# Performance work log

Hardware: AMD Instinct MI355X
Metric: run time of the kernel (lower is better)

The kernel has to match this reference:

```python
import jax, jax.numpy as jnp
import numpy as np

D_MODEL = 256
D_INNER = 512   # expand * dim
D_STATE = 16
D_CONV = 4
DT_RANK = 16    # ceil(dim / 16)
PATCH = 64


def _silu(v):
    return v * jax.nn.sigmoid(v)


def _causal_dwconv(x, w, b):
    # x: (b, d, l); w: (d, 1, k) depthwise; causal left pad k-1
    y = jax.lax.conv_general_dilated(
        x, w, window_strides=(1,), padding=[(D_CONV - 1, 0)],
        feature_group_count=D_INNER, dimension_numbers=("NCH", "OIH", "NCH"))
    return y + b[None, :, None]


def _selective_scan(u, delta, A, Bm, Cm, Dp):
    # u, delta: (b, d, l); A: (d, n); Bm, Cm: (b, n, l)
    dA = jnp.exp(jnp.einsum("bdl,dn->lbdn", delta, A))
    dBu = jnp.einsum("bdl,bnl,bdl->lbdn", delta, Bm, u)
    Ct = jnp.transpose(Cm, (2, 0, 1))  # (l, b, n)

    def step(h, inp):
        dA_t, dBu_t, c_t = inp
        h = dA_t * h + dBu_t
        return h, jnp.einsum("bdn,bn->bd", h, c_t)

    h0 = jnp.zeros(u.shape[:2] + (A.shape[1],), u.dtype)
    _, ys = jax.lax.scan(step, h0, (dA, dBu, Ct))  # ys: (l, b, d)
    return jnp.transpose(ys, (1, 2, 0)) + Dp[None, :, None] * u


def _mamba_branch(xz, conv_w, conv_b, xproj_w, dtp_w, dtp_b, A_log, Dp):
    xpart, z = jnp.split(xz, 2, axis=1)  # each (b, d_inner, l)
    xc = _silu(_causal_dwconv(xpart, conv_w, conv_b))
    xdbl = jnp.einsum("bdl,ed->bel", xc, xproj_w)  # e = dt_rank + 2*d_state
    dt = xdbl[:, :DT_RANK]
    Bm = xdbl[:, DT_RANK:DT_RANK + D_STATE]
    Cm = xdbl[:, DT_RANK + D_STATE:]
    delta = jax.nn.softplus(jnp.einsum("brl,dr->bdl", dt, dtp_w) + dtp_b[None, :, None])
    A = -jnp.exp(A_log)
    y = _selective_scan(xc, delta, A, Bm, Cm, Dp)
    return y * _silu(z)


def setup_inputs():
    key = jax.random.key(0)
    ks = jax.random.split(key, 16)

    def nrm(k, shape, s=0.02):
        return jax.random.normal(k, shape, jnp.float32) * s

    A_init = jnp.log(jnp.tile(jnp.arange(1, D_STATE + 1, dtype=jnp.float32), (D_INNER, 1)))
    return {
        "x": jax.random.normal(ks[0], (2, D_MODEL, 4096), jnp.float32),
        "ln_g": jnp.ones((D_MODEL,), jnp.float32),
        "ln_b": jnp.zeros((D_MODEL,), jnp.float32),
        "in_proj_w": nrm(ks[1], (2 * D_INNER, D_MODEL)),
        "conv_w": nrm(ks[2], (D_INNER, 1, D_CONV), 0.1),
        "conv_b": nrm(ks[3], (D_INNER,), 0.01),
        "x_proj_w": nrm(ks[4], (DT_RANK + 2 * D_STATE, D_INNER)),
        "dt_proj_w": nrm(ks[5], (D_INNER, DT_RANK), 0.1),
        "dt_proj_b": nrm(ks[6], (D_INNER,), 0.1),
        "A_log": A_init,
        "D_f": jnp.ones((D_INNER,), jnp.float32),
        "conv_w_b": nrm(ks[7], (D_INNER, 1, D_CONV), 0.1),
        "conv_b_b": nrm(ks[8], (D_INNER,), 0.01),
        "x_proj_w_b": nrm(ks[9], (DT_RANK + 2 * D_STATE, D_INNER)),
        "dt_proj_w_b": nrm(ks[10], (D_INNER, DT_RANK), 0.1),
        "dt_proj_b_b": nrm(ks[11], (D_INNER,), 0.1),
        "A_b_log": A_init,
        "D_b": jnp.ones((D_INNER,), jnp.float32),
        "out_proj_w": nrm(ks[12], (D_MODEL, D_INNER)),
        "depth": 4,
    }


def reference(x, ln_g, ln_b, in_proj_w, conv_w, conv_b, x_proj_w, dt_proj_w,
              dt_proj_b, A_log, D_f, conv_w_b, conv_b_b, x_proj_w_b,
              dt_proj_w_b, dt_proj_b_b, A_b_log, D_b, out_proj_w, depth):
    assert depth in (3, 4, 5)
    B, C, L = x.shape
    ps = PATCH
    xp, Lp = x, L
    if L % ps != 0:  # borrow-pad (static shape logic, mirrors torch code)
        pad_len = ps - L % ps
        start = max(L - L % ps - pad_len, 0)
        xp = jnp.concatenate([x, x[:, :, start:start + pad_len]], axis=2)
        Lp = L + pad_len
    npt = Lp // ps
    # (B, C, npt, ps) -> (B*ps, C, npt) -> (B*ps, npt, C)
    xd = xp.reshape(B, C, npt, ps).transpose(0, 3, 1, 2).reshape(B * ps, C, npt)
    xf = jnp.transpose(xd, (0, 2, 1))
    # LayerNorm over channel dim
    mu = xf.mean(-1, keepdims=True)
    var = ((xf - mu) ** 2).mean(-1, keepdims=True)
    xn = (xf - mu) * jax.lax.rsqrt(var + 1e-5) * ln_g + ln_b
    # in_proj -> (b, 2*d_inner, l)
    xz = jnp.einsum("blc,ec->bel", xn, in_proj_w)
    y_f = _mamba_branch(xz, conv_w, conv_b, x_proj_w, dt_proj_w, dt_proj_b, A_log, D_f)
    y_b = _mamba_branch(xz[:, :, ::-1], conv_w_b, conv_b_b, x_proj_w_b,
                        dt_proj_w_b, dt_proj_b_b, A_b_log, D_b)[:, :, ::-1]
    y = y_f + y_b
    out_m = jnp.einsum("bdl,cd->blc", y, out_proj_w)  # (B*ps, npt, C)
    # mirrors torch: reshape(B, ps, npt, C).permute(0,3,1,2).reshape(B, C, Lp)
    xo = out_m.reshape(B, ps, npt, C).transpose(0, 3, 1, 2).reshape(B, C, Lp)
    xo = xo[:, :, :L]
    return xo + x
```

## Files before the change

### kernel.cpp

```cpp
#include <hip/hip_runtime.h>


#define OFF_XZ 0
#define OFF_XC 8388608
#define OFF_DL 12582912
#define OFF_BC 16777216
#define OFF_YF 17039360
#define OFF_YB 19136512
#define OFF_WOB 21233664

typedef __attribute__((ext_vector_type(8))) short short8;
typedef __attribute__((ext_vector_type(4))) float f32x4;

__device__ __forceinline__ float siluf(float v) {
    return v / (1.f + __expf(-v));
}
__device__ __forceinline__ float softplusf(float v) {
    return (v > 20.f) ? v : log1pf(__expf(v));
}
__device__ __forceinline__ unsigned short f2bf(float f) {
    union { float f; unsigned int u; } v; v.f = f;
    unsigned int u = v.u;
    return (unsigned short)((u + 0x7FFFu + ((u >> 16) & 1u)) >> 16);
}

__global__ __launch_bounds__(256) void k_cvt_w(
    const float* __restrict__ W, unsigned short* __restrict__ Wb, int n4)
{
    int i = blockIdx.x * 256 + threadIdx.x;
    if (i >= n4) return;
    float4 v = *(const float4*)(W + i * 4);
    ushort4 o;
    o.x = f2bf(v.x); o.y = f2bf(v.y); o.z = f2bf(v.z); o.w = f2bf(v.w);
    *(ushort4*)(Wb + i * 4) = o;
}

__global__ __launch_bounds__(256) void k_ln_inproj_mfma(
    const float* __restrict__ x, const float* __restrict__ g,
    const float* __restrict__ bt, const unsigned short* __restrict__ Wb,
    float* __restrict__ xz)
{
    __shared__ unsigned short sxb[64 * 256];
    const int bid = blockIdx.x;
    const int pg = bid >> 2, og = bid & 3;
    const int p0 = pg * 64;
    const int tid = threadIdx.x;
    const int wave = tid >> 6, lane = tid & 63;
    const int b = pg >> 6, pp = pg & 63;
    const float* xb = x + ((size_t)b * 256) * 4096 + pp;

    const int c = lane * 4;
    const float g0 = g[c + 0], g1 = g[c + 1], g2 = g[c + 2], g3 = g[c + 3];
    const float b0 = bt[c + 0], b1 = bt[c + 1], b2 = bt[c + 2], b3 = bt[c + 3];
    for (int i = 0; i < 16; ++i) {
        int m = wave * 16 + i;
        const float* xr = xb + m * 64;
        float v0 = xr[(size_t)(c + 0) * 4096];
        float v1 = xr[(size_t)(c + 1) * 4096];
        float v2 = xr[(size_t)(c + 2) * 4096];
        float v3 = xr[(size_t)(c + 3) * 4096];
        float s = v0 + v1 + v2 + v3;
        #pragma unroll
        for (int o = 32; o; o >>= 1) s += __shfl_xor(s, o);
        float mu = s * (1.f / 256.f);
        float q0 = v0 - mu, q1 = v1 - mu, q2 = v2 - mu, q3 = v3 - mu;
        float q = q0 * q0 + q1 * q1 + q2 * q2 + q3 * q3;
        #pragma unroll
        for (int o = 32; o; o >>= 1) q += __shfl_xor(q, o);
        float rs = rsqrtf(q * (1.f / 256.f) + 1e-5f);
        ushort4 pk;
        pk.x = f2bf(q0 * rs * g0 + b0);
        pk.y = f2bf(q1 * rs * g1 + b1);
        pk.z = f2bf(q2 * rs * g2 + b2);
        pk.w = f2bf(q3 * rs * g3 + b3);
        int byte = m * 512 + lane * 8;
        byte ^= (m & 7) << 4;
        *(ushort4*)((char*)sxb + byte) = pk;
    }
    __syncthreads();

    const int nbase = og * 256 + wave * 64;
    const int l15 = lane & 15, lg = lane >> 4;
    f32x4 acc[4][4];
    #pragma unroll
    for (int mi = 0; mi < 4; ++mi)
        #pragma unroll
        for (int ni = 0; ni < 4; ++ni) acc[mi][ni] = (f32x4){0.f, 0.f, 0.f, 0.f};

    const unsigned short* wrow[4];
    #pragma unroll
    for (int ni = 0; ni < 4; ++ni)
        wrow[ni] = Wb + (size_t)(nbase + ni * 16 + l15) * 256 + lg * 8;

    #pragma unroll 2
    for (int k0 = 0; k0 < 256; k0 += 32) {
        short8 a[4], bfr[4];
        #pragma unroll
        for (int mi = 0; mi < 4; ++mi) {
            int row = mi * 16 + l15;
            int byte = row * 512 + k0 * 2 + lg * 16;
            byte ^= (row & 7) << 4;
            a[mi] = *(const short8*)((const char*)sxb + byte);
        }
        #pragma unroll
        for (int ni = 0; ni < 4; ++ni)
            bfr[ni] = *(const short8*)(wrow[ni] + k0);
        #pragma unroll
        for (int mi = 0; mi < 4; ++mi)
            #pragma unroll
            for (int ni = 0; ni < 4; ++ni)
                acc[mi][ni] = __builtin_amdgcn_mfma_f32_16x16x32_bf16(
                    a[mi], bfr[ni], acc[mi][ni], 0, 0, 0);
    }

    #pragma unroll
    for (int mi = 0; mi < 4; ++mi)
        #pragma unroll
        for (int ni = 0; ni < 4; ++ni)
            #pragma unroll
            for (int r = 0; r < 4; ++r)
                xz[(size_t)(p0 + mi * 16 + lg * 4 + r) * 1024 + nbase + ni * 16 + l15] =
                    acc[mi][ni][r];
}

__global__ __launch_bounds__(256) void k_cxdt(
    const float* __restrict__ xz, const float* __restrict__ cw,
    const float* __restrict__ cb, const float* __restrict__ W6,
    const float* __restrict__ dtw, const float* __restrict__ dtb,
    float* __restrict__ xc, float* __restrict__ delta,
    float* __restrict__ bcb, int rev)
{
    __shared__ float sx2[16][516];
    __shared__ float sdtw[16][512];
    __shared__ float sdbl[16][48];
    const int blk = blockIdx.x;
    const int bp  = blk >> 2;
    const int i0  = (blk & 3) << 4;
    const int tid = threadIdx.x;

    #pragma unroll
    for (int q = 0; q < 8; ++q) {
        int f4 = q * 256 + tid;
        int d = f4 >> 2, r0 = (f4 & 3) * 4;
        float4 w = *(const float4*)(dtw + d * 16 + r0);
        sdtw[r0 + 0][d] = w.x;
        sdtw[r0 + 1][d] = w.y;
        sdtw[r0 + 2][d] = w.z;
        sdtw[r0 + 3][d] = w.w;
    }

    const size_t xzrow = (size_t)bp * 64;
    #pragma unroll
    for (int half = 0; half < 2; ++half) {
        int d = half * 256 + tid;
        float w0 = cw[d * 4 + 0], w1 = cw[d * 4 + 1], w2 = cw[d * 4 + 2], w3 = cw[d * 4 + 3];
        float bb = cb[d];
        float p1 = 0.f, p2 = 0.f, p3 = 0.f;
        if (i0 > 0) {
            p1 = xz[(xzrow + (rev ? 63 - (i0 - 1) : i0 - 1)) * 1024 + d];
            p2 = xz[(xzrow + (rev ? 63 - (i0 - 2) : i0 - 2)) * 1024 + d];
            p3 = xz[(xzrow + (rev ? 63 - (i0 - 3) : i0 - 3)) * 1024 + d];
        }
        for (int p = 0; p < 16; ++p) {
            int i = i0 + p;
            int l = rev ? 63 - i : i;
            float cur = xz[(xzrow + l) * 1024 + d];
            float y = w3 * cur + w2 * p1 + w1 * p2 + w0 * p3 + bb;
            float s = siluf(y);
            sx2[p][d] = s;
            xc[(xzrow + i) * 512 + d] = s;
            p3 = p2; p2 = p1; p1 = cur;
        }
    }
    __syncthreads();

    #pragma unroll
    for (int k = 0; k < 3; ++k) {
        int o = k * 256 + tid;
        int e = o >> 4, p = o & 15;
        const float4* wr = (const float4*)(W6 + (size_t)e * 512);
        float a = 0.f;
        for (int c4 = 0; c4 < 128; ++c4) {
            float4 w = wr[c4];
            float4 xv = *(const float4*)&sx2[p][c4 * 4];
            a = fmaf(w.x, xv.x, a); a = fmaf(w.y, xv.y, a);
            a = fmaf(w.z, xv.z, a); a = fmaf(w.w, xv.w, a);
        }
        sdbl[p][e] = a;
    }
    __syncthreads();

    #pragma unroll
    for (int k = 0; k < 32; ++k) {
        int o = k * 256 + tid;
        int p = o >> 9, d = o & 511;
        float a = dtb[d];
        #pragma unroll
        for (int r = 0; r < 16; ++r)
            a = fmaf(sdtw[r][d], sdbl[p][r], a);
        delta[(xzrow + i0 + p) * 512 + d] = softplusf(a);
    }
    #pragma unroll
    for (int k = 0; k < 2; ++k) {
        int o = k * 256 + tid;
        int p = o >> 5, n = o & 31;
        bcb[(xzrow + i0 + p) * 32 + n] = sdbl[p][16 + n];
    }
}

__global__ __launch_bounds__(256) void k_scan(
    const float* __restrict__ delta, const float* __restrict__ u_,
    const float* __restrict__ bc_, const float* __restrict__ xz,
    const float* __restrict__ A_log, const float* __restrict__ Dp,
    unsigned short* __restrict__ yout, int rev)
{
    const int bid = blockIdx.x;
    const int bp  = bid >> 1;
    const int d   = ((bid & 1) << 8) + threadIdx.x;

    float a[16];
    #pragma unroll
    for (int n = 0; n < 16; ++n) a[n] = -__expf(A_log[(size_t)d * 16 + n]);
    const float Dd = Dp[d];

    float h[16];
    #pragma unroll
    for (int n = 0; n < 16; ++n) h[n] = 0.f;

    for (int l = 0; l < 64; ++l) {
        size_t base = (size_t)bp * 64 + l;
        float dl = delta[base * 512 + d];
        float uu = u_[base * 512 + d];
        float du = dl * uu;
        const float4* bc = (const float4*)(bc_ + base * 32);
        float y = 0.f;
        #pragma unroll
        for (int n4 = 0; n4 < 4; ++n4) {
            float4 Bv = bc[n4];
            float4 Cv = bc[4 + n4];
            int n = n4 * 4;
            h[n + 0] = fmaf(__expf(dl * a[n + 0]), h[n + 0], du * Bv.x); y = fmaf(h[n + 0], Cv.x, y);
            h[n + 1] = fmaf(__expf(dl * a[n + 1]), h[n + 1], du * Bv.y); y = fmaf(h[n + 1], Cv.y, y);
            h[n + 2] = fmaf(__expf(dl * a[n + 2]), h[n + 2], du * Bv.z); y = fmaf(h[n + 2], Cv.z, y);
            h[n + 3] = fmaf(__expf(dl * a[n + 3]), h[n + 3], du * Bv.w); y = fmaf(h[n + 3], Cv.w, y);
        }
        y = fmaf(Dd, uu, y);
        int lo = rev ? 63 - l : l;
        float zv = xz[((size_t)bp * 64 + lo) * 1024 + 512 + d];
        yout[((size_t)bp * 64 + lo) * 512 + d] = f2bf(y * siluf(zv));
    }
}

__global__ __launch_bounds__(256) void k_outproj_mfma(
    const unsigned short* __restrict__ yf, const unsigned short* __restrict__ yb,
    const unsigned short* __restrict__ wob, const float* __restrict__ x,
    float* __restrict__ out)
{
    __shared__ float sD[64][257];
    const int blk = blockIdx.x;
    const int g = blk >> 6, l = blk & 63;
    const int tid = threadIdx.x;
    const int wave = tid >> 6, lane = tid & 63;
    const int l15 = lane & 15, lg = lane >> 4;
    const int cbase = wave * 64;

    f32x4 acc[4][4];
    #pragma unroll
    for (int mi = 0; mi < 4; ++mi)
        #pragma unroll
        for (int ni = 0; ni < 4; ++ni) acc[mi][ni] = (f32x4){0.f, 0.f, 0.f, 0.f};

    const unsigned short* arf[4];
    const unsigned short* arb[4];
    #pragma unroll
    for (int mi = 0; mi < 4; ++mi) {
        size_t idx = (((size_t)(g * 64 + mi * 16 + l15)) * 64 + l) * 512 + lg * 8;
        arf[mi] = yf + idx;
        arb[mi] = yb + idx;
    }
    const unsigned short* brow[4];
    #pragma unroll
    for (int ni = 0; ni < 4; ++ni)
        brow[ni] = wob + (size_t)(cbase + ni * 16 + l15) * 512 + lg * 8;

    #pragma unroll 2
    for (int k0 = 0; k0 < 512; k0 += 32) {
        short8 bw[4], af[4], ab[4];
        #pragma unroll
        for (int ni = 0; ni < 4; ++ni) bw[ni] = *(const short8*)(brow[ni] + k0);
        #pragma unroll
        for (int mi = 0; mi < 4; ++mi) {
            af[mi] = *(const short8*)(arf[mi] + k0);
            ab[mi] = *(const short8*)(arb[mi] + k0);
        }
        #pragma unroll
        for (int mi = 0; mi < 4; ++mi)
            #pragma unroll
            for (int ni = 0; ni < 4; ++ni) {
                acc[mi][ni] = __builtin_amdgcn_mfma_f32_16x16x32_bf16(
                    af[mi], bw[ni], acc[mi][ni], 0, 0, 0);
                acc[mi][ni] = __builtin_amdgcn_mfma_f32_16x16x32_bf16(
                    ab[mi], bw[ni], acc[mi][ni], 0, 0, 0);
            }
    }

    #pragma unroll
    for (int mi = 0; mi < 4; ++mi)
        #pragma unroll
        for (int ni = 0; ni < 4; ++ni)
            #pragma unroll
            for (int r = 0; r < 4; ++r)
                sD[mi * 16 + lg * 4 + r][cbase + ni * 16 + l15] = acc[mi][ni][r];
    __syncthreads();

    #pragma unroll
    for (int q = 0; q < 16; ++q) {
        int f4 = q * 256 + tid;
        int cc = f4 >> 4, m4 = f4 & 15;
        size_t idx = ((size_t)(g * 256 + cc)) * 4096 + (size_t)l * 64 + m4 * 4;
        float4 xr = *(const float4*)(x + idx);
        float4 v;
        v.x = sD[m4 * 4 + 0][cc] + xr.x;
        v.y = sD[m4 * 4 + 1][cc] + xr.y;
        v.z = sD[m4 * 4 + 2][cc] + xr.z;
        v.w = sD[m4 * 4 + 3][cc] + xr.w;
        *(float4*)(out + idx) = v;
    }
}

extern "C" void kernel_launch(void* const* d_in, const int* in_sizes, int n_in,
                              void* d_out, int out_size, void* d_ws, size_t ws_size,
                              hipStream_t stream) {
    const float* x        = (const float*)d_in[0];
    const float* ln_g     = (const float*)d_in[1];
    const float* ln_b     = (const float*)d_in[2];
    const float* in_w     = (const float*)d_in[3];
    const float* conv_w   = (const float*)d_in[4];
    const float* conv_b   = (const float*)d_in[5];
    const float* xproj_w  = (const float*)d_in[6];
    const float* dtp_w    = (const float*)d_in[7];
    const float* dtp_b    = (const float*)d_in[8];
    const float* A_log    = (const float*)d_in[9];
    const float* D_f      = (const float*)d_in[10];
    const float* conv_w_b = (const float*)d_in[11];
    const float* conv_b_b = (const float*)d_in[12];
    const float* xproj_wb = (const float*)d_in[13];
    const float* dtp_w_b  = (const float*)d_in[14];
    const float* dtp_b_b  = (const float*)d_in[15];
    const float* A_b_log  = (const float*)d_in[16];
    const float* D_b      = (const float*)d_in[17];
    const float* out_w    = (const float*)d_in[18];
    float* out = (float*)d_out;

    float* ws  = (float*)d_ws;
    float* xz  = ws + OFF_XZ;
    float* xc  = ws + OFF_XC;
    float* dl  = ws + OFF_DL;
    float* bc  = ws + OFF_BC;
    unsigned short* w_bf = (unsigned short*)(ws + OFF_BC);
    unsigned short* yf   = (unsigned short*)(ws + OFF_YF);
    unsigned short* yb   = (unsigned short*)(ws + OFF_YB);
    unsigned short* wob  = (unsigned short*)(ws + OFF_WOB);

    k_cvt_w<<<256, 256, 0, stream>>>(in_w, w_bf, 65536);
    k_cvt_w<<<128, 256, 0, stream>>>(out_w, wob, 32768);
    k_ln_inproj_mfma<<<512, 256, 0, stream>>>(x, ln_g, ln_b, w_bf, xz);
    k_cxdt<<<512, 256, 0, stream>>>(xz, conv_w, conv_b, xproj_w, dtp_w, dtp_b,
                                    xc, dl, bc, 0);
    k_scan<<<256, 256, 0, stream>>>(dl, xc, bc, xz, A_log, D_f, yf, 0);
    k_cxdt<<<512, 256, 0, stream>>>(xz, conv_w_b, conv_b_b, xproj_wb, dtp_w_b, dtp_b_b,
                                    xc, dl, bc, 1);
    k_scan<<<256, 256, 0, stream>>>(dl, xc, bc, xz, A_b_log, D_b, yb, 1);
    k_outproj_mfma<<<128, 256, 0, stream>>>(yf, yb, wob, x, out);
}
```

Before: 351.5 us.

## Fold dt_proj into x_proj weights and compute delta/B/C with bf16 MFMA

Precomputes a combined weight matrix (dt_proj_w @ x_proj_w[:16] for the delta rows, plus the B/C rows of x_proj) in bf16. The conv+silu kernel then stores a full 64-position bf16 tile in swizzled LDS and runs a single MFMA GEMM producing delta (with softplus) and B/C directly. This replaces the scalar fp32 x_proj dot products and the separate dt_proj FMA loop, but adds a weight-prep kernel per direction and bf16 rounding of both activations and the folded weights.

```diff
diff --git a/kernel.cpp b/kernel.cpp
--- a/kernel.cpp
+++ b/kernel.cpp
@@ -8,6 +8,7 @@
 #define OFF_YF 17039360
 #define OFF_YB 19136512
 #define OFF_WOB 21233664
+#define OFF_WX 21299200
 
 typedef __attribute__((ext_vector_type(8))) short short8;
 typedef __attribute__((ext_vector_type(4))) float f32x4;
@@ -33,6 +34,29 @@
     ushort4 o;
     o.x = f2bf(v.x); o.y = f2bf(v.y); o.z = f2bf(v.z); o.w = f2bf(v.w);
     *(ushort4*)(Wb + i * 4) = o;
+}
+
+__global__ __launch_bounds__(256) void k_mk_wx(
+    const float* __restrict__ W6, const float* __restrict__ dtw,
+    unsigned short* __restrict__ Wx)
+{
+    const int n = blockIdx.x;
+    const int c = threadIdx.x;
+    if (n < 512) {
+        float a0 = 0.f, a1 = 0.f;
+        #pragma unroll
+        for (int r = 0; r < 16; ++r) {
+            float w = dtw[n * 16 + r];
+            a0 = fmaf(w, W6[r * 512 + c], a0);
+            a1 = fmaf(w, W6[r * 512 + c + 256], a1);
+        }
+        Wx[n * 512 + c] = f2bf(a0);
+        Wx[n * 512 + c + 256] = f2bf(a1);
+    } else {
+        int rr = n - 496;
+        Wx[n * 512 + c] = f2bf(W6[rr * 512 + c]);
+        Wx[n * 512 + c + 256] = f2bf(W6[rr * 512 + c + 256]);
+    }
 }
 
 __global__ __launch_bounds__(256) void k_ln_inproj_mfma(
@@ -123,88 +147,112 @@
                     acc[mi][ni][r];
 }
 
-__global__ __launch_bounds__(256) void k_cxdt(
+__global__ __launch_bounds__(256) void k_cxg(
     const float* __restrict__ xz, const float* __restrict__ cw,
-    const float* __restrict__ cb, const float* __restrict__ W6,
-    const float* __restrict__ dtw, const float* __restrict__ dtb,
+    const float* __restrict__ cb, const unsigned short* __restrict__ Wx,
+    const float* __restrict__ dtb,
     float* __restrict__ xc, float* __restrict__ delta,
     float* __restrict__ bcb, int rev)
 {
-    __shared__ float sx2[16][516];
-    __shared__ float sdtw[16][512];
-    __shared__ float sdbl[16][48];
+    __shared__ unsigned short sxb[64 * 512];
     const int blk = blockIdx.x;
-    const int bp  = blk >> 2;
-    const int i0  = (blk & 3) << 4;
+    const int bp = blk >> 1, og = blk & 1;
     const int tid = threadIdx.x;
-
-    #pragma unroll
-    for (int q = 0; q < 8; ++q) {
-        int f4 = q * 256 + tid;
-        int d = f4 >> 2, r0 = (f4 & 3) * 4;
-        float4 w = *(const float4*)(dtw + d * 16 + r0);
-        sdtw[r0 + 0][d] = w.x;
-        sdtw[r0 + 1][d] = w.y;
-        sdtw[r0 + 2][d] = w.z;
-        sdtw[r0 + 3][d] = w.w;
-    }
-
+    const int wave = tid >> 6, lane = tid & 63;
     const size_t xzrow = (size_t)bp * 64;
-    #pragma unroll
-    for (int half = 0; half < 2; ++half) {
-        int d = half * 256 + tid;
-        float w0 = cw[d * 4 + 0], w1 = cw[d * 4 + 1], w2 = cw[d * 4 + 2], w3 = cw[d * 4 + 3];
-        float bb = cb[d];
-        float p1 = 0.f, p2 = 0.f, p3 = 0.f;
-        if (i0 > 0) {
-            p1 = xz[(xzrow + (rev ? 63 - (i0 - 1) : i0 - 1)) * 1024 + d];
-            p2 = xz[(xzrow + (rev ? 63 - (i0 - 2) : i0 - 2)) * 1024 + d];
-            p3 = xz[(xzrow + (rev ? 63 - (i0 - 3) : i0 - 3)) * 1024 + d];
+    const int m0 = wave * 16;
+
+    {
+        const int da = lane * 4, db = 256 + lane * 4;
+        float4 wa0 = *(const float4*)&cw[(da + 0) * 4];
+        float4 wa1 = *(const float4*)&cw[(da + 1) * 4];
+        float4 wa2 = *(const float4*)&cw[(da + 2) * 4];
+        float4 wa3 = *(const float4*)&cw[(da + 3) * 4];
+        float4 wb0 = *(const float4*)&cw[(db + 0) * 4];
+        float4 wb1 = *(const float4*)&cw[(db + 1) * 4];
+        float4 wb2 = *(const float4*)&cw[(db + 2) * 4];
+        float4 wb3 = *(const float4*)&cw[(db + 3) * 4];
+        float4 ba = *(const float4*)&cb[da];
+        float4 bb = *(const float4*)&cb[db];
+
+        float4 a1 = {0,0,0,0}, a2 = {0,0,0,0}, a3 = {0,0,0,0};
+        float4 c1 = {0,0,0,0}, c2 = {0,0,0,0}, c3 = {0,0,0,0};
+        if (m0 > 0) {
+            int i1 = m0 - 1, i2 = m0 - 2, i3 = m0 - 3;
+            int l1 = rev ? 63 - i1 : i1, l2 = rev ? 63 - i2 : i2, l3 = rev ? 63 - i3 : i3;
+            a1 = *(const float4*)&xz[(xzrow + l1) * 1024 + da];
+            a2 = *(const float4*)&xz[(xzrow + l2) * 1024 + da];
+            a3 = *(const float4*)&xz[(xzrow + l3) * 1024 + da];
+            c1 = *(const float4*)&xz[(xzrow + l1) * 1024 + db];
+            c2 = *(const float4*)&xz[(xzrow + l2) * 1024 + db];
+            c3 = *(const float4*)&xz[(xzrow + l3) * 1024 + db];
         }
         for (int p = 0; p < 16; ++p) {
-            int i = i0 + p;
+            int i = m0 + p;
             int l = rev ? 63 - i : i;
-            float cur = xz[(xzrow + l) * 1024 + d];
-            float y = w3 * cur + w2 * p1 + w1 * p2 + w0 * p3 + bb;
-            float s = siluf(y);
-            sx2[p][d] = s;
-            xc[(xzrow + i) * 512 + d] = s;
-            p3 = p2; p2 = p1; p1 = cur;
+            float4 cura = *(const float4*)&xz[(xzrow + l) * 1024 + da];
+            float4 curb = *(const float4*)&xz[(xzrow + l) * 1024 + db];
+            float4 sa, sb;
+            sa.x = siluf(wa0.w * cura.x + wa0.z * a1.x + wa0.y * a2.x + wa0.x * a3.x + ba.x);
+            sa.y = siluf(wa1.w * cura.y + wa1.z * a1.y + wa1.y * a2.y + wa1.x * a3.y + ba.y);
+            sa.z = siluf(wa2.w * cura.z + wa2.z * a1.z + wa2.y * a2.z + wa2.x * a3.z + ba.z);
+            sa.w = siluf(wa3.w * cura.w + wa3.z * a1.w + wa3.y * a2.w + wa3.x * a3.w + ba.w);
+            sb.x = siluf(wb0.w * curb.x + wb0.z * c1.x + wb0.y * c2.x + wb0.x * c3.x + bb.x);
+            sb.y = siluf(wb1.w * curb.y + wb1.z * c1.y + wb1.y * c2.y + wb1.x * c3.y + bb.y);
+            sb.z = siluf(wb2.w * curb.z + wb2.z * c1.z + wb2.y * c2.z + wb2.x * c3.z + bb.z);
+            sb.w = siluf(wb3.w * curb.w + wb3.z * c1.w + wb3.y * c2.w + wb3.x * c3.w + bb.w);
+            if (og == 0) {
+                *(float4*)&xc[(xzrow + i) * 512 + da] = sa;
+                *(float4*)&xc[(xzrow + i) * 512 + db] = sb;
+            }
+            ushort4 pa, pb;
+            pa.x = f2bf(sa.x); pa.y = f2bf(sa.y); pa.z = f2bf(sa.z); pa.w = f2bf(sa.w);
+            pb.x = f2bf(sb.x); pb.y = f2bf(sb.y); pb.z = f2bf(sb.z); pb.w = f2bf(sb.w);
+            int bytea = i * 1024 + da * 2; bytea ^= (i & 7) << 4;
+            int byteb = i * 1024 + db * 2; byteb ^= (i & 7) << 4;
+            *(ushort4*)((char*)sxb + bytea) = pa;
+            *(ushort4*)((char*)sxb + byteb) = pb;
+            a3 = a2; a2 = a1; a1 = cura;
+            c3 = c2; c2 = c1; c1 = curb;
         }
     }
     __syncthreads();
 
-    #pragma unroll
-    for (int k = 0; k < 3; ++k) {
-        int o = k * 256 + tid;
-        int e = o >> 4, p = o & 15;
-        const float4* wr = (const float4*)(W6 + (size_t)e * 512);
-        float a = 0.f;
-        for (int c4 = 0; c4 < 128; ++c4) {
-            float4 w = wr[c4];
-            float4 xv = *(const float4*)&sx2[p][c4 * 4];
-            a = fmaf(w.x, xv.x, a); a = fmaf(w.y, xv.y, a);
-            a = fmaf(w.z, xv.z, a); a = fmaf(w.w, xv.w, a);
-        }
-        sdbl[p][e] = a;
-    }
-    __syncthreads();
-
-    #pragma unroll
-    for (int k = 0; k < 32; ++k) {
-        int o = k * 256 + tid;
-        int p = o >> 9, d = o & 511;
-        float a = dtb[d];
-        #pragma unroll
-        for (int r = 0; r < 16; ++r)
-            a = fmaf(sdtw[r][d], sdbl[p][r], a);
-        delta[(xzrow + i0 + p) * 512 + d] = softplusf(a);
-    }
-    #pragma unroll
-    for (int k = 0; k < 2; ++k) {
-        int o = k * 256 + tid;
-        int p = o >> 5, n = o & 31;
-        bcb[(xzrow + i0 + p) * 32 + n] = sdbl[p][16 + n];
+    const int l15 = lane & 15, lg = lane >> 4;
+    f32x4 acc[17];
+    #pragma unroll
+    for (int ni = 0; ni < 17; ++ni) acc[ni] = (f32x4){0.f, 0.f, 0.f, 0.f};
+    const unsigned short* bbase = Wx + (size_t)(og * 272 + l15) * 512 + lg * 8;
+    const int arow = m0 + l15;
+    const int abase = arow * 1024 + lg * 16;
+    const int aswz = (arow & 7) << 4;
+
+    for (int k0 = 0; k0 < 512; k0 += 32) {
+        short8 af = *(const short8*)((const char*)sxb + ((abase + k0 * 2) ^ aswz));
+        #pragma unroll
+        for (int ni = 0; ni < 17; ++ni) {
+            short8 bw = *(const short8*)(bbase + (size_t)ni * 8192 + k0);
+            acc[ni] = __builtin_amdgcn_mfma_f32_16x16x32_bf16(af, bw, acc[ni], 0, 0, 0);
+        }
+    }
+
+    #pragma unroll
+    for (int ni = 0; ni < 17; ++ni) {
+        int col = og * 272 + ni * 16 + l15;
+        if (col < 512) {
+            float bias = dtb[col];
+            #pragma unroll
+            for (int r = 0; r < 4; ++r) {
+                int pos = m0 + lg * 4 + r;
+                delta[(xzrow + pos) * 512 + col] = softplusf(acc[ni][r] + bias);
+            }
+        } else {
+            #pragma unroll
+            for (int r = 0; r < 4; ++r) {
+                int pos = m0 + lg * 4 + r;
+                bcb[(xzrow + pos) * 32 + (col - 512)] = acc[ni][r];
+            }
+        }
     }
 }
 
@@ -361,15 +409,16 @@
     unsigned short* yf   = (unsigned short*)(ws + OFF_YF);
     unsigned short* yb   = (unsigned short*)(ws + OFF_YB);
     unsigned short* wob  = (unsigned short*)(ws + OFF_WOB);
+    unsigned short* wx   = (unsigned short*)(ws + OFF_WX);
 
     k_cvt_w<<<256, 256, 0, stream>>>(in_w, w_bf, 65536);
     k_cvt_w<<<128, 256, 0, stream>>>(out_w, wob, 32768);
     k_ln_inproj_mfma<<<512, 256, 0, stream>>>(x, ln_g, ln_b, w_bf, xz);
-    k_cxdt<<<512, 256, 0, stream>>>(xz, conv_w, conv_b, xproj_w, dtp_w, dtp_b,
-                                    xc, dl, bc, 0);
+    k_mk_wx<<<544, 256, 0, stream>>>(xproj_w, dtp_w, wx);
+    k_cxg<<<256, 256, 0, stream>>>(xz, conv_w, conv_b, wx, dtp_b, xc, dl, bc, 0);
     k_scan<<<256, 256, 0, stream>>>(dl, xc, bc, xz, A_log, D_f, yf, 0);
-    k_cxdt<<<512, 256, 0, stream>>>(xz, conv_w_b, conv_b_b, xproj_wb, dtp_w_b, dtp_b_b,
-                                    xc, dl, bc, 1);
+    k_mk_wx<<<544, 256, 0, stream>>>(xproj_wb, dtp_w_b, wx);
+    k_cxg<<<256, 256, 0, stream>>>(xz, conv_w_b, conv_b_b, wx, dtp_b_b, xc, dl, bc, 1);
     k_scan<<<256, 256, 0, stream>>>(dl, xc, bc, xz, A_b_log, D_b, yb, 1);
     k_outproj_mfma<<<128, 256, 0, stream>>>(yf, yb, wob, x, out);
 }
```

New measurement: 394.5 us. 1.12x slower.
